# Optimization experiments

Measured on AMD Instinct MI355X. Metric: run time of the kernel, lower is better.

Reference implementation:

```python
import jax, jax.numpy as jnp
import numpy as np


def setup_inputs() -> dict:
    key = jax.random.key(0)
    ks = jax.random.split(key, 8)
    b, n, d = 4, 4096, 64
    scale = 1.0 / np.sqrt(d)
    return {
        "x": jax.random.normal(ks[0], (b, n, d), jnp.float32),
        "W1": jax.random.normal(ks[1], (d, d), jnp.float32) * scale,
        "b1": jax.random.normal(ks[2], (d,), jnp.float32) * 0.01,
        "W2": jax.random.normal(ks[3], (d, d), jnp.float32) * scale,
        "b2": jax.random.normal(ks[4], (d,), jnp.float32) * 0.01,
        "W3": jax.random.normal(ks[5], (d, d), jnp.float32) * scale,
        "b3": jax.random.normal(ks[6], (d,), jnp.float32) * 0.01,
        "temperature": jnp.array(4.0, jnp.float32),  # nn.Parameter init
        "k": 8,
    }


def reference(x, W1, b1, W2, b2, W3, b3, temperature, k):
    b, n, d = x.shape
    # MLP projection (torch Linear: y = x @ W.T + b)
    h = jax.nn.relu(x @ W1.T + b1)
    h = jax.nn.relu(h @ W2.T + b2)
    h = h @ W3.T + b3  # [b, n, d]

    tau = jnp.exp(jnp.clip(temperature, -5.0, 5.0))

    # pairwise squared euclidean distances [b, n, n]
    sq = jnp.sum(h * h, axis=-1)  # [b, n]
    dist = sq[:, :, None] + sq[:, None, :] - 2.0 * jnp.einsum("bnd,bmd->bnm", h, h)

    # argKmin over j (keops dim=1 reduction): k smallest scaled distances per row i
    _, idx = jax.lax.top_k(-(dist * tau), k)  # idx [b, n, k]

    idx_flat = idx.reshape(b, n * k)
    # gather neighbor features and recompute distances (as in the original)
    x1 = jnp.take_along_axis(h, idx_flat[:, :, None], axis=1)  # [b, n*k, d]
    x2 = jnp.repeat(h, k, axis=1)  # [b, n*k, d]
    dng = jnp.sum((x1 - x2) ** 2, axis=-1)  # [b, n*k]
    logprobs = (-dng * tau).reshape(b, n, k)

    rows = jnp.broadcast_to(jnp.arange(n)[None, :, None], (b, n, k)).reshape(b, n * k)
    edges = jnp.stack((idx_flat, rows), axis=-1)  # [b, n*k, 2]
    return edges, logprobs
```

## Files before the change

### kernel.cpp

```cpp
#include <hip/hip_runtime.h>
#include <math.h>

#define BB 4
#define NN 4096
#define DD 64
#define KK 8
#define CH 4
#define NT ((NN / CH) / 64)

#if defined(__has_builtin)
#if __has_builtin(__builtin_amdgcn_fmed3f)
#define FMED3(a, x, b) __builtin_amdgcn_fmed3f((x), (a), (b))
#endif
#endif
#ifndef FMED3
#define FMED3(a, x, b) fminf(fmaxf((a), (x)), (b))
#endif

__device__ __forceinline__ float tau_of(const float* __restrict__ temp) {
  float tc = temp[0];
  tc = fminf(fmaxf(tc, -5.0f), 5.0f);
  return expf(tc);
}

__device__ __forceinline__ void ins_med3(float (&kk)[KK], int (&kj)[KK], float key, int j) {
  const bool l0 = key < kk[0], l1 = key < kk[1], l2 = key < kk[2], l3 = key < kk[3];
  const bool l4 = key < kk[4], l5 = key < kk[5], l6 = key < kk[6], l7 = key < kk[7];
  kj[7] = l6 ? kj[6] : (l7 ? j : kj[7]);  kk[7] = FMED3(kk[6], key, kk[7]);
  kj[6] = l5 ? kj[5] : (l6 ? j : kj[6]);  kk[6] = FMED3(kk[5], key, kk[6]);
  kj[5] = l4 ? kj[4] : (l5 ? j : kj[5]);  kk[5] = FMED3(kk[4], key, kk[5]);
  kj[4] = l3 ? kj[3] : (l4 ? j : kj[4]);  kk[4] = FMED3(kk[3], key, kk[4]);
  kj[3] = l2 ? kj[2] : (l3 ? j : kj[3]);  kk[3] = FMED3(kk[2], key, kk[3]);
  kj[2] = l1 ? kj[1] : (l2 ? j : kj[2]);  kk[2] = FMED3(kk[1], key, kk[2]);
  kj[1] = l0 ? kj[0] : (l1 ? j : kj[1]);  kk[1] = FMED3(kk[0], key, kk[1]);
  kj[0] = l0 ? j : kj[0];                 kk[0] = fminf(kk[0], key);
}

__device__ __forceinline__ void ins_lex(float (&kk)[KK], int (&kj)[KK], float key, int j) {
  if (key < kk[KK - 1] || (key == kk[KK - 1] && j < kj[KK - 1])) {
    kk[KK - 1] = key; kj[KK - 1] = j;
#pragma unroll
    for (int m = KK - 1; m > 0; --m) {
      bool sw = (kk[m] < kk[m - 1]) || (kk[m] == kk[m - 1] && kj[m] < kj[m - 1]);
      if (sw) {
        float tk = kk[m]; kk[m] = kk[m - 1]; kk[m - 1] = tk;
        int tj = kj[m]; kj[m] = kj[m - 1]; kj[m - 1] = tj;
      }
    }
  }
}

__device__ __forceinline__ void scatter16(float (*dst)[64], int dc, int col,
                                          const float4& a, const float4& b,
                                          const float4& c, const float4& d) {
  dst[dc + 0][col] = a.x; dst[dc + 1][col] = a.y; dst[dc + 2][col] = a.z; dst[dc + 3][col] = a.w;
  dst[dc + 4][col] = b.x; dst[dc + 5][col] = b.y; dst[dc + 6][col] = b.z; dst[dc + 7][col] = b.w;
  dst[dc + 8][col] = c.x; dst[dc + 9][col] = c.y; dst[dc + 10][col] = c.z; dst[dc + 11][col] = c.w;
  dst[dc + 12][col] = d.x; dst[dc + 13][col] = d.y; dst[dc + 14][col] = d.z; dst[dc + 15][col] = d.w;
}

__device__ __forceinline__ void mlp_layer(const float (*bin)[68], float (*bout)[68],
                                          float (*wT)[68], float* bias,
                                          const float* __restrict__ Wg,
                                          const float* __restrict__ bg,
                                          bool dorelu, int t) {
  const int rr = t >> 2;
  const int dc = (t & 3) << 4;
  {
    const float* wsrc = Wg + rr * DD + dc;
#pragma unroll
    for (int q = 0; q < 16; ++q) wT[dc + q][rr] = wsrc[q];
    if (t < DD) bias[t] = bg[t];
  }
  __syncthreads();
  const int tg = t & 15, og = t >> 4;
  float acc[4][4];
#pragma unroll
  for (int r = 0; r < 4; ++r)
#pragma unroll
    for (int c = 0; c < 4; ++c) acc[r][c] = 0.f;
#pragma unroll 4
  for (int i = 0; i < DD; ++i) {
    const float4 av = *reinterpret_cast<const float4*>(&bin[i][tg << 2]);
    const float4 wv = *reinterpret_cast<const float4*>(&wT[i][og << 2]);
    float aa[4] = {av.x, av.y, av.z, av.w};
    float ww[4] = {wv.x, wv.y, wv.z, wv.w};
#pragma unroll
    for (int r = 0; r < 4; ++r)
#pragma unroll
      for (int c = 0; c < 4; ++c) acc[r][c] += aa[r] * ww[c];
  }
#pragma unroll
  for (int r = 0; r < 4; ++r)
#pragma unroll
    for (int c = 0; c < 4; ++c) {
      float v = acc[r][c] + bias[(og << 2) + c];
      if (dorelu) v = fmaxf(v, 0.f);
      bout[(og << 2) + c][(tg << 2) + r] = v;
    }
  __syncthreads();
}

__global__ __launch_bounds__(256) void k_mlp(
    const float* __restrict__ x,
    const float* __restrict__ W1, const float* __restrict__ b1,
    const float* __restrict__ W2, const float* __restrict__ b2,
    const float* __restrict__ W3, const float* __restrict__ b3,
    float* __restrict__ h, float* __restrict__ sqo) {
  __shared__ float bufA[DD][68];
  __shared__ float bufB[DD][68];
  __shared__ float wT[DD][68];
  __shared__ float bias[DD];
  const int t = threadIdx.x;
  const size_t tok0 = (size_t)blockIdx.x * 64;
  const int rr = t >> 2;
  const int dc = (t & 3) << 4;
  {
    const float* src = x + (tok0 + rr) * DD + dc;
#pragma unroll
    for (int q = 0; q < 16; ++q) bufA[dc + q][rr] = src[q];
  }
  mlp_layer(bufA, bufB, wT, bias, W1, b1, true, t);
  mlp_layer(bufB, bufA, wT, bias, W2, b2, true, t);
  mlp_layer(bufA, bufB, wT, bias, W3, b3, false, t);
  {
    float s = 0.f;
    float* dst = h + (tok0 + rr) * DD + dc;
#pragma unroll
    for (int q = 0; q < 16; ++q) {
      float v = bufB[dc + q][rr];
      dst[q] = v;
      s += v * v;
    }
    s += __shfl_xor(s, 1);
    s += __shfl_xor(s, 2);
    if ((t & 3) == 0) sqo[tok0 + rr] = s;
  }
}

__global__ __launch_bounds__(256, 3) void k_disttopk(
    const float* __restrict__ h, const float* __restrict__ sq,
    const float* __restrict__ temp,
    float* __restrict__ pk, int* __restrict__ pj) {
  __shared__ __align__(16) char smem[16384 + 16384 + 256];
  float (*hiT)[64] = (float (*)[64])(smem);
  float (*hjT)[64] = (float (*)[64])(smem + 16384);
  float* sqjS = (float*)(smem + 32768);

  const int t = threadIdx.x;
  const int bx = blockIdx.x;
  const int b = bx >> 8;
  const int rem = bx & 255;
  const int rt = rem >> 2;
  const int ch = rem & 3;
  const int i0 = rt << 6;
  const int jbase = ch * (NN / CH);
  const float* hb = h + (size_t)b * NN * DD;
  const float* sqb = sq + b * NN;
  const float tau = tau_of(temp);

  const int rg = t >> 3;
  const int cg = t & 7;
  const int r0 = rg << 1;
  const int c0 = cg << 3;
  const int rr = t >> 2;
  const int dc = (t & 3) << 4;

  {
    const float* src = hb + (size_t)(i0 + rr) * DD + dc;
    float4 f0 = *(const float4*)(src);
    float4 f1 = *(const float4*)(src + 4);
    float4 f2 = *(const float4*)(src + 8);
    float4 f3 = *(const float4*)(src + 12);
    scatter16(hiT, dc, rr, f0, f1, f2, f3);
  }
  {
    const float* src = hb + (size_t)(jbase + rr) * DD + dc;
    float4 f0 = *(const float4*)(src);
    float4 f1 = *(const float4*)(src + 4);
    float4 f2 = *(const float4*)(src + 8);
    float4 f3 = *(const float4*)(src + 12);
    scatter16(hjT, dc, rr, f0, f1, f2, f3);
    if (t < 64) sqjS[t] = sqb[jbase + t];
  }
  const float sqi0 = sqb[i0 + r0];
  const float sqi1 = sqb[i0 + r0 + 1];

  float kkA[KK]; int kjA[KK];
  float kkB[KK]; int kjB[KK];
#pragma unroll
  for (int m = 0; m < KK; ++m) {
    kkA[m] = 3.0e38f; kjA[m] = 0x7fffffff;
    kkB[m] = 3.0e38f; kjB[m] = 0x7fffffff;
  }

  __syncthreads();

  for (int jt = 0; jt < NT; ++jt) {
    const int j0 = jbase + (jt << 6);

    float4 pf0, pf1, pf2, pf3; float psq = 0.f;
    const bool hasNext = (jt + 1 < NT);
    if (hasNext) {
      const float* src = hb + (size_t)(j0 + 64 + rr) * DD + dc;
      pf0 = *(const float4*)(src);
      pf1 = *(const float4*)(src + 4);
      pf2 = *(const float4*)(src + 8);
      pf3 = *(const float4*)(src + 12);
      if (t < 64) psq = sqb[j0 + 64 + t];
    }

    float acc[2][8];
#pragma unroll
    for (int r = 0; r < 2; ++r)
#pragma unroll
      for (int c = 0; c < 8; ++c) acc[r][c] = 0.f;
#pragma unroll 8
    for (int d = 0; d < DD; ++d) {
      const float2 a2 = *(const float2*)(&hiT[d][r0]);
      const float4 b0 = *(const float4*)(&hjT[d][c0]);
      const float4 b1 = *(const float4*)(&hjT[d][c0 + 4]);
      float bb[8] = {b0.x, b0.y, b0.z, b0.w, b1.x, b1.y, b1.z, b1.w};
#pragma unroll
      for (int c = 0; c < 8; ++c) {
        acc[0][c] += a2.x * bb[c];
        acc[1][c] += a2.y * bb[c];
      }
    }
    const float4 sj0 = *(const float4*)(&sqjS[c0]);
    const float4 sj1 = *(const float4*)(&sqjS[c0 + 4]);
    float sj[8] = {sj0.x, sj0.y, sj0.z, sj0.w, sj1.x, sj1.y, sj1.z, sj1.w};
#pragma unroll
    for (int c = 0; c < 8; ++c) {
      const int j = j0 + c0 + c;
      float keyA = __fmul_rn(__builtin_fmaf(-2.0f, acc[0][c], __fadd_rn(sqi0, sj[c])), tau);
      ins_med3(kkA, kjA, keyA, j);
      float keyB = __fmul_rn(__builtin_fmaf(-2.0f, acc[1][c], __fadd_rn(sqi1, sj[c])), tau);
      ins_med3(kkB, kjB, keyB, j);
    }
    __syncthreads();
    if (hasNext) {
      scatter16(hjT, dc, rr, pf0, pf1, pf2, pf3);
      if (t < 64) sqjS[t] = psq;
    }
    __syncthreads();
  }

  float* dK = (float*)(smem);
  int*   dJ = (int*)(smem + 16384);
#pragma unroll
  for (int m = 0; m < KK; ++m) {
    dK[(r0 * 8 + cg) * KK + m] = kkA[m];
    dJ[(r0 * 8 + cg) * KK + m] = kjA[m];
    dK[((r0 + 1) * 8 + cg) * KK + m] = kkB[m];
    dJ[((r0 + 1) * 8 + cg) * KK + m] = kjB[m];
  }
  __syncthreads();

  float fk[KK]; int fj[KK];
#pragma unroll
  for (int m = 0; m < KK; ++m) { fk[m] = 3.0e38f; fj[m] = 0x7fffffff; }
  const int rowA = t >> 1, half = t & 1;
  if (t < 128) {
#pragma unroll
    for (int o = 0; o < 4; ++o) {
#pragma unroll
      for (int m = 0; m < KK; ++m) {
        ins_lex(fk, fj, dK[(rowA * 8 + half * 4 + o) * KK + m],
                        dJ[(rowA * 8 + half * 4 + o) * KK + m]);
      }
    }
  }
  __syncthreads();
  float* oK = (float*)(smem);
  int*   oJ = (int*)(smem + 4096);
  if (t < 128) {
#pragma unroll
    for (int m = 0; m < KK; ++m) {
      oK[(rowA * 2 + half) * KK + m] = fk[m];
      oJ[(rowA * 2 + half) * KK + m] = fj[m];
    }
  }
  __syncthreads();

  if (t < 64) {
    float gk[KK]; int gj[KK];
#pragma unroll
    for (int m = 0; m < KK; ++m) { gk[m] = 3.0e38f; gj[m] = 0x7fffffff; }
#pragma unroll
    for (int q = 0; q < 2; ++q) {
#pragma unroll
      for (int m = 0; m < KK; ++m) {
        ins_lex(gk, gj, oK[(t * 2 + q) * KK + m], oJ[(t * 2 + q) * KK + m]);
      }
    }
    const size_t base = ((size_t)(b * NN + i0 + t) * CH + ch) * KK;
#pragma unroll
    for (int m = 0; m < KK; ++m) { pk[base + m] = gk[m]; pj[base + m] = gj[m]; }
  }
}

__global__ __launch_bounds__(256) void k_final(
    const float* __restrict__ h, const float* __restrict__ pk,
    const int* __restrict__ pj, const float* __restrict__ temp,
    float* __restrict__ out) {
  const int gid = blockIdx.x * 256 + threadIdx.x;
  const int b = gid >> 12;
  const int i = gid & (NN - 1);
  const float tau = tau_of(temp);

  float fk[KK]; int fj[KK];
#pragma unroll
  for (int m = 0; m < KK; ++m) { fk[m] = 3.0e38f; fj[m] = 0x7fffffff; }
  const size_t base = (size_t)(b * NN + i) * CH * KK;
#pragma unroll
  for (int s = 0; s < CH * KK; ++s) {
    ins_lex(fk, fj, pk[base + s], pj[base + s]);
  }

  const float* hi = h + (size_t)(b * NN + i) * DD;
  float4 xi[16];
#pragma unroll
  for (int q = 0; q < 16; ++q) xi[q] = *reinterpret_cast<const float4*>(hi + (q << 2));

  float* oute = out;
  float* outl = out + (size_t)BB * NN * KK * 2;
#pragma unroll
  for (int m = 0; m < KK; ++m) {
    const int j = fj[m];
    const float* hj = h + (size_t)(b * NN + j) * DD;
    float dng = 0.f;
#pragma unroll
    for (int q = 0; q < 16; ++q) {
      const float4 vj = *reinterpret_cast<const float4*>(hj + (q << 2));
      float dx = xi[q].x - vj.x; dng += dx * dx;
      float dy = xi[q].y - vj.y; dng += dy * dy;
      float dz = xi[q].z - vj.z; dng += dz * dz;
      float dw = xi[q].w - vj.w; dng += dw * dw;
    }
    const size_t e = (size_t)(b * NN + i) * KK + m;
    oute[e * 2 + 0] = (float)j;
    oute[e * 2 + 1] = (float)i;
    outl[e] = -__fmul_rn(dng, tau);
  }
}

extern "C" void kernel_launch(void* const* d_in, const int* in_sizes, int n_in,
                              void* d_out, int out_size, void* d_ws, size_t ws_size,
                              hipStream_t stream) {
  const float* x  = (const float*)d_in[0];
  const float* W1 = (const float*)d_in[1];
  const float* b1 = (const float*)d_in[2];
  const float* W2 = (const float*)d_in[3];
  const float* b2 = (const float*)d_in[4];
  const float* W3 = (const float*)d_in[5];
  const float* b3 = (const float*)d_in[6];
  const float* temp = (const float*)d_in[7];
  (void)in_sizes; (void)n_in; (void)out_size; (void)ws_size;

  float* ws = (float*)d_ws;
  float* h  = ws;
  float* sq = h + (size_t)BB * NN * DD;
  float* pk = sq + (size_t)BB * NN;
  int*   pj = (int*)(pk + (size_t)BB * NN * CH * KK);
  float* out = (float*)d_out;

  k_mlp<<<BB * NN / 64, 256, 0, stream>>>(x, W1, b1, W2, b2, W3, b3, h, sq);
  k_disttopk<<<BB * (NN / 64) * CH, 256, 0, stream>>>(h, sq, temp, pk, pj);
  k_final<<<BB * NN / 256, 256, 0, stream>>>(h, pk, pj, temp, out);
}
```

Baseline: 301.3 us.

## Enlarge distance tile to 128 query rows with 4x8 register blocking

The distance/top-k kernel now processes 128 query rows per block instead of 64, so each thread computes a 4x8 register tile rather than 2x8. This halves the number of times each j tile is loaded from global memory and raises FMA work per shared-memory read. The per-row top-k merge is done in two passes through a new merge64 helper to fit the existing shared buffers. In exchange it uses more registers (four top-k lists per thread) and more shared memory, and launches half as many blocks, which may lower occupancy under the 3-blocks launch bound.

```diff
diff --git a/kernel.cpp b/kernel.cpp
--- a/kernel.cpp
+++ b/kernel.cpp
@@ -7,6 +7,7 @@
 #define KK 8
 #define CH 4
 #define NT ((NN / CH) / 64)
+#define IT 128
 
 #if defined(__has_builtin)
 #if __has_builtin(__builtin_amdgcn_fmed3f)
@@ -50,13 +51,11 @@
   }
 }
 
-__device__ __forceinline__ void scatter16(float (*dst)[64], int dc, int col,
-                                          const float4& a, const float4& b,
-                                          const float4& c, const float4& d) {
-  dst[dc + 0][col] = a.x; dst[dc + 1][col] = a.y; dst[dc + 2][col] = a.z; dst[dc + 3][col] = a.w;
-  dst[dc + 4][col] = b.x; dst[dc + 5][col] = b.y; dst[dc + 6][col] = b.z; dst[dc + 7][col] = b.w;
-  dst[dc + 8][col] = c.x; dst[dc + 9][col] = c.y; dst[dc + 10][col] = c.z; dst[dc + 11][col] = c.w;
-  dst[dc + 12][col] = d.x; dst[dc + 13][col] = d.y; dst[dc + 14][col] = d.z; dst[dc + 15][col] = d.w;
+__device__ __forceinline__ void scat4i(float (*dst)[IT], int d0, int col, const float4& v) {
+  dst[d0 + 0][col] = v.x; dst[d0 + 1][col] = v.y; dst[d0 + 2][col] = v.z; dst[d0 + 3][col] = v.w;
+}
+__device__ __forceinline__ void scat4j(float (*dst)[64], int d0, int col, const float4& v) {
+  dst[d0 + 0][col] = v.x; dst[d0 + 1][col] = v.y; dst[d0 + 2][col] = v.z; dst[d0 + 3][col] = v.w;
 }
 
 __device__ __forceinline__ void mlp_layer(const float (*bin)[68], float (*bout)[68],
@@ -138,22 +137,68 @@
   }
 }
 
+__device__ __forceinline__ void merge64(char* smem, int t, int rowOff,
+                                        int b, int i0, int ch,
+                                        float* __restrict__ pk, int* __restrict__ pj) {
+  float* dK = (float*)(smem);
+  int*   dJ = (int*)(smem + 16384);
+  float* oK = (float*)(smem);
+  int*   oJ = (int*)(smem + 4096);
+  __syncthreads();
+  float fk[KK]; int fj[KK];
+#pragma unroll
+  for (int m = 0; m < KK; ++m) { fk[m] = 3.0e38f; fj[m] = 0x7fffffff; }
+  const int rowA = t >> 1, half = t & 1;
+  if (t < 128) {
+#pragma unroll
+    for (int o = 0; o < 4; ++o)
+#pragma unroll
+      for (int m = 0; m < KK; ++m)
+        ins_lex(fk, fj, dK[(rowA * 8 + half * 4 + o) * KK + m],
+                        dJ[(rowA * 8 + half * 4 + o) * KK + m]);
+  }
+  __syncthreads();
+  if (t < 128) {
+#pragma unroll
+    for (int m = 0; m < KK; ++m) {
+      oK[(rowA * 2 + half) * KK + m] = fk[m];
+      oJ[(rowA * 2 + half) * KK + m] = fj[m];
+    }
+  }
+  __syncthreads();
+  if (t < 64) {
+    float gk[KK]; int gj[KK];
+#pragma unroll
+    for (int m = 0; m < KK; ++m) { gk[m] = 3.0e38f; gj[m] = 0x7fffffff; }
+#pragma unroll
+    for (int q = 0; q < 2; ++q)
+#pragma unroll
+      for (int m = 0; m < KK; ++m)
+        ins_lex(gk, gj, oK[(t * 2 + q) * KK + m], oJ[(t * 2 + q) * KK + m]);
+    const int grow = ((t >> 1) << 2) + (t & 1) + rowOff;
+    const size_t base = ((size_t)(b * NN + i0 + grow) * CH + ch) * KK;
+#pragma unroll
+    for (int m = 0; m < KK; ++m) { pk[base + m] = gk[m]; pj[base + m] = gj[m]; }
+  }
+  __syncthreads();
+}
+
 __global__ __launch_bounds__(256, 3) void k_disttopk(
     const float* __restrict__ h, const float* __restrict__ sq,
     const float* __restrict__ temp,
     float* __restrict__ pk, int* __restrict__ pj) {
-  __shared__ __align__(16) char smem[16384 + 16384 + 256];
-  float (*hiT)[64] = (float (*)[64])(smem);
-  float (*hjT)[64] = (float (*)[64])(smem + 16384);
-  float* sqjS = (float*)(smem + 32768);
+  __shared__ __align__(16) char smem[32768 + 16384 + 256];
+  float (*hiT)[IT] = (float (*)[IT])(smem);
+  float (*hjT)[64] = (float (*)[64])(smem + 32768);
+  float* sqjS = (float*)(smem + 49152);
 
   const int t = threadIdx.x;
   const int bx = blockIdx.x;
-  const int b = bx >> 8;
-  const int rem = bx & 255;
+  const int b = bx >> 7;
+  const int rem = bx & 127;
   const int rt = rem >> 2;
   const int ch = rem & 3;
-  const int i0 = rt << 6;
+  const int i0 = rt << 7;
   const int jbase = ch * (NN / CH);
   const float* hb = h + (size_t)b * NN * DD;
   const float* sqb = sq + b * NN;
@@ -161,37 +206,51 @@
 
   const int rg = t >> 3;
   const int cg = t & 7;
-  const int r0 = rg << 1;
+  const int r0 = rg << 2;
   const int c0 = cg << 3;
-  const int rr = t >> 2;
-  const int dc = (t & 3) << 4;
-
-  {
-    const float* src = hb + (size_t)(i0 + rr) * DD + dc;
-    float4 f0 = *(const float4*)(src);
-    float4 f1 = *(const float4*)(src + 4);
-    float4 f2 = *(const float4*)(src + 8);
-    float4 f3 = *(const float4*)(src + 12);
-    scatter16(hiT, dc, rr, f0, f1, f2, f3);
-  }
-  {
-    const float* src = hb + (size_t)(jbase + rr) * DD + dc;
-    float4 f0 = *(const float4*)(src);
-    float4 f1 = *(const float4*)(src + 4);
-    float4 f2 = *(const float4*)(src + 8);
-    float4 f3 = *(const float4*)(src + 12);
-    scatter16(hjT, dc, rr, f0, f1, f2, f3);
+  const int tokJ = t & 63;
+  const int dhJ = (t >> 6) << 4;
+
+  {
+    const int tok = t & 127;
+    const int dh = (t >> 7) << 5;
+    const float* src = hb + (size_t)(i0 + tok) * DD + dh;
+    const float4 g0 = *(const float4*)(src);
+    const float4 g1 = *(const float4*)(src + 4);
+    const float4 g2 = *(const float4*)(src + 8);
+    const float4 g3 = *(const float4*)(src + 12);
+    const float4 g4 = *(const float4*)(src + 16);
+    const float4 g5 = *(const float4*)(src + 20);
+    const float4 g6 = *(const float4*)(src + 24);
+    const float4 g7 = *(const float4*)(src + 28);
+    scat4i(hiT, dh + 0, tok, g0);  scat4i(hiT, dh + 4, tok, g1);
+    scat4i(hiT, dh + 8, tok, g2);  scat4i(hiT, dh + 12, tok, g3);
+    scat4i(hiT, dh + 16, tok, g4); scat4i(hiT, dh + 20, tok, g5);
+    scat4i(hiT, dh + 24, tok, g6); scat4i(hiT, dh + 28, tok, g7);
+  }
+  {
+    const float* src = hb + (size_t)(jbase + tokJ) * DD + dhJ;
+    const float4 g0 = *(const float4*)(src);
+    const float4 g1 = *(const float4*)(src + 4);
+    const float4 g2 = *(const float4*)(src + 8);
+    const float4 g3 = *(const float4*)(src + 12);
+    scat4j(hjT, dhJ + 0, tokJ, g0);  scat4j(hjT, dhJ + 4, tokJ, g1);
+    scat4j(hjT, dhJ + 8, tokJ, g2);  scat4j(hjT, dhJ + 12, tokJ, g3);
     if (t < 64) sqjS[t] = sqb[jbase + t];
   }
-  const float sqi0 = sqb[i0 + r0];
+  const float sqi0 = sqb[i0 + r0 + 0];
   const float sqi1 = sqb[i0 + r0 + 1];
-
-  float kkA[KK]; int kjA[KK];
-  float kkB[KK]; int kjB[KK];
+  const float sqi2 = sqb[i0 + r0 + 2];
+  const float sqi3 = sqb[i0 + r0 + 3];
+
+  float kk0[KK], kk1[KK], kk2[KK], kk3[KK];
+  int kj0[KK], kj1[KK], kj2[KK], kj3[KK];
 #pragma unroll
   for (int m = 0; m < KK; ++m) {
-    kkA[m] = 3.0e38f; kjA[m] = 0x7fffffff;
-    kkB[m] = 3.0e38f; kjB[m] = 0x7fffffff;
+    kk0[m] = 3.0e38f; kj0[m] = 0x7fffffff;
+    kk1[m] = 3.0e38f; kj1[m] = 0x7fffffff;
+    kk2[m] = 3.0e38f; kj2[m] = 0x7fffffff;
+    kk3[m] = 3.0e38f; kj3[m] = 0x7fffffff;
   }
 
   __syncthreads();
@@ -202,7 +261,7 @@
     float4 pf0, pf1, pf2, pf3; float psq = 0.f;
     const bool hasNext = (jt + 1 < NT);
     if (hasNext) {
-      const float* src = hb + (size_t)(j0 + 64 + rr) * DD + dc;
+      const float* src = hb + (size_t)(j0 + 64 + tokJ) * DD + dhJ;
       pf0 = *(const float4*)(src);
       pf1 = *(const float4*)(src + 4);
       pf2 = *(const float4*)(src + 8);
@@ -210,94 +269,73 @@
       if (t < 64) psq = sqb[j0 + 64 + t];
     }
 
-    float acc[2][8];
-#pragma unroll
-    for (int r = 0; r < 2; ++r)
+    float acc[4][8];
+#pragma unroll
+    for (int r = 0; r < 4; ++r)
 #pragma unroll
       for (int c = 0; c < 8; ++c) acc[r][c] = 0.f;
-#pragma unroll 8
+#pragma unroll 4
     for (int d = 0; d < DD; ++d) {
-      const float2 a2 = *(const float2*)(&hiT[d][r0]);
+      const float4 av = *(const float4*)(&hiT[d][r0]);
       const float4 b0 = *(const float4*)(&hjT[d][c0]);
       const float4 b1 = *(const float4*)(&hjT[d][c0 + 4]);
-      float bb[8] = {b0.x, b0.y, b0.z, b0.w, b1.x, b1.y, b1.z, b1.w};
-#pragma unroll
-      for (int c = 0; c < 8; ++c) {
-        acc[0][c] += a2.x * bb[c];
-        acc[1][c] += a2.y * bb[c];
-      }
+      const float aa[4] = {av.x, av.y, av.z, av.w};
+      const float bb[8] = {b0.x, b0.y, b0.z, b0.w, b1.x, b1.y, b1.z, b1.w};
+#pragma unroll
+      for (int r = 0; r < 4; ++r)
+#pragma unroll
+        for (int c = 0; c < 8; ++c) acc[r][c] += aa[r] * bb[c];
     }
     const float4 sj0 = *(const float4*)(&sqjS[c0]);
     const float4 sj1 = *(const float4*)(&sqjS[c0 + 4]);
-    float sj[8] = {sj0.x, sj0.y, sj0.z, sj0.w, sj1.x, sj1.y, sj1.z, sj1.w};
+    const float sj[8] = {sj0.x, sj0.y, sj0.z, sj0.w, sj1.x, sj1.y, sj1.z, sj1.w};
 #pragma unroll
     for (int c = 0; c < 8; ++c) {
       const int j = j0 + c0 + c;
-      float keyA = __fmul_rn(__builtin_fmaf(-2.0f, acc[0][c], __fadd_rn(sqi0, sj[c])), tau);
-      ins_med3(kkA, kjA, keyA, j);
-      float keyB = __fmul_rn(__builtin_fmaf(-2.0f, acc[1][c], __fadd_rn(sqi1, sj[c])), tau);
-      ins_med3(kkB, kjB, keyB, j);
+      float k0 = __fmul_rn(__builtin_fmaf(-2.0f, acc[0][c], __fadd_rn(sqi0, sj[c])), tau);
+      ins_med3(kk0, kj0, k0, j);
+      float k1 = __fmul_rn(__builtin_fmaf(-2.0f, acc[1][c], __fadd_rn(sqi1, sj[c])), tau);
+      ins_med3(kk1, kj1, k1, j);
+      float k2 = __fmul_rn(__builtin_fmaf(-2.0f, acc[2][c], __fadd_rn(sqi2, sj[c])), tau);
+      ins_med3(kk2, kj2, k2, j);
+      float k3 = __fmul_rn(__builtin_fmaf(-2.0f, acc[3][c], __fadd_rn(sqi3, sj[c])), tau);
+      ins_med3(kk3, kj3, k3, j);
     }
     __syncthreads();
     if (hasNext) {
-      scatter16(hjT, dc, rr, pf0, pf1, pf2, pf3);
+      scat4j(hjT, dhJ + 0, tokJ, pf0);  scat4j(hjT, dhJ + 4, tokJ, pf1);
+      scat4j(hjT, dhJ + 8, tokJ, pf2);  scat4j(hjT, dhJ + 12, tokJ, pf3);
       if (t < 64) sqjS[t] = psq;
     }
     __syncthreads();
   }
 
-  float* dK = (float*)(smem);
-  int*   dJ = (int*)(smem + 16384);
-#pragma unroll
-  for (int m = 0; m < KK; ++m) {
-    dK[(r0 * 8 + cg) * KK + m] = kkA[m];
-    dJ[(r0 * 8 + cg) * KK + m] = kjA[m];
-    dK[((r0 + 1) * 8 + cg) * KK + m] = kkB[m];
-    dJ[((r0 + 1) * 8 + cg) * KK + m] = kjB[m];
-  }
-  __syncthreads();
-
-  float fk[KK]; int fj[KK];
-#pragma unroll
-  for (int m = 0; m < KK; ++m) { fk[m] = 3.0e38f; fj[m] = 0x7fffffff; }
-  const int rowA = t >> 1, half = t & 1;
-  if (t < 128) {
-#pragma unroll
-    for (int o = 0; o < 4; ++o) {
-#pragma unroll
-      for (int m = 0; m < KK; ++m) {
-        ins_lex(fk, fj, dK[(rowA * 8 + half * 4 + o) * KK + m],
-                        dJ[(rowA * 8 + half * 4 + o) * KK + m]);
-      }
-    }
-  }
-  __syncthreads();
-  float* oK = (float*)(smem);
-  int*   oJ = (int*)(smem + 4096);
-  if (t < 128) {
+  {
+    float* dK = (float*)(smem);
+    int*   dJ = (int*)(smem + 16384);
+    const int lr = rg << 1;
 #pragma unroll
     for (int m = 0; m < KK; ++m) {
-      oK[(rowA * 2 + half) * KK + m] = fk[m];
-      oJ[(rowA * 2 + half) * KK + m] = fj[m];
-    }
-  }
-  __syncthreads();
-
-  if (t < 64) {
-    float gk[KK]; int gj[KK];
-#pragma unroll
-    for (int m = 0; m < KK; ++m) { gk[m] = 3.0e38f; gj[m] = 0x7fffffff; }
-#pragma unroll
-    for (int q = 0; q < 2; ++q) {
-#pragma unroll
-      for (int m = 0; m < KK; ++m) {
-        ins_lex(gk, gj, oK[(t * 2 + q) * KK + m], oJ[(t * 2 + q) * KK + m]);
-      }
-    }
-    const size_t base = ((size_t)(b * NN + i0 + t) * CH + ch) * KK;
-#pragma unroll
-    for (int m = 0; m < KK; ++m) { pk[base + m] = gk[m]; pj[base + m] = gj[m]; }
-  }
+      dK[((lr + 0) * 8 + cg) * KK + m] = kk0[m];
+      dJ[((lr + 0) * 8 + cg) * KK + m] = kj0[m];
+      dK[((lr + 1) * 8 + cg) * KK + m] = kk1[m];
+      dJ[((lr + 1) * 8 + cg) * KK + m] = kj1[m];
+    }
+  }
+  merge64(smem, t, 0, b, i0, ch, pk, pj);
+  {
+    float* dK = (float*)(smem);
+    int*   dJ = (int*)(smem + 16384);
+    const int lr = rg << 1;
+#pragma unroll
+    for (int m = 0; m < KK; ++m) {
+      dK[((lr + 0) * 8 + cg) * KK + m] = kk2[m];
+      dJ[((lr + 0) * 8 + cg) * KK + m] = kj2[m];
+      dK[((lr + 1) * 8 + cg) * KK + m] = kk3[m];
+      dJ[((lr + 1) * 8 + cg) * KK + m] = kj3[m];
+    }
+  }
+  merge64(smem, t, 2, b, i0, ch, pk, pj);
 }
 
 __global__ __launch_bounds__(256) void k_final(
@@ -366,6 +404,6 @@
   float* out = (float*)d_out;
 
   k_mlp<<<BB * NN / 64, 256, 0, stream>>>(x, W1, b1, W2, b2, W3, b3, h, sq);
-  k_disttopk<<<BB * (NN / 64) * CH, 256, 0, stream>>>(h, sq, temp, pk, pj);
+  k_disttopk<<<BB * (NN / IT) * CH, 256, 0, stream>>>(h, sq, temp, pk, pj);
   k_final<<<BB * NN / 256, 256, 0, stream>>>(h, pk, pj, temp, out);
 }
```

After: 364.8 us. +21.1%, slower.
